# Kernel tuning notes

Hardware: AMD Instinct MI355X
Metric: run time of the kernel (lower is better)

The kernel has to match this reference:

```python
import jax, jax.numpy as jnp
import numpy as np

EMBED_DIM = 1024
NUM_HEADS = 16
HEAD_DIM = EMBED_DIM // NUM_HEADS


def setup_inputs() -> dict:
    key = jax.random.key(0)
    k1, k2, k3, k4 = jax.random.split(key, 4)
    S, B = 2048, 2
    x = jax.random.normal(k1, (S, B, EMBED_DIM), dtype=jnp.float32)
    # xavier_uniform for in_proj_weight [3E, E]
    limit_in = float(np.sqrt(6.0 / (3 * EMBED_DIM + EMBED_DIM)))
    in_proj_weight = jax.random.uniform(k2, (3 * EMBED_DIM, EMBED_DIM), minval=-limit_in, maxval=limit_in, dtype=jnp.float32)
    in_proj_bias = jnp.zeros((3 * EMBED_DIM,), dtype=jnp.float32)
    # out_proj: nn.Linear default init (kaiming-uniform-ish); use uniform of similar scale
    limit_out = float(np.sqrt(1.0 / EMBED_DIM))
    out_proj_weight = jax.random.uniform(k3, (EMBED_DIM, EMBED_DIM), minval=-limit_out, maxval=limit_out, dtype=jnp.float32)
    out_proj_bias = jnp.zeros((EMBED_DIM,), dtype=jnp.float32)
    return {
        "x": x,
        "in_proj_weight": in_proj_weight,
        "in_proj_bias": in_proj_bias,
        "out_proj_weight": out_proj_weight,
        "out_proj_bias": out_proj_bias,
    }


def reference(x, in_proj_weight, in_proj_bias, out_proj_weight, out_proj_bias):
    S, B, E = x.shape
    H, D = NUM_HEADS, HEAD_DIM
    scaling = float(D) ** -0.5
    # fused QKV projection: [S, B, 3E]
    qkv = jnp.einsum("sbe,fe->sbf", x, in_proj_weight) + in_proj_bias
    q, k, v = jnp.split(qkv, 3, axis=-1)
    q = q * scaling
    # [S, B, E] -> [B*H, S, D]
    def to_heads(t):
        return t.reshape(S, B * H, D).transpose(1, 0, 2)
    q, k, v = to_heads(q), to_heads(k), to_heads(v)
    # attention scores [B*H, S, S]
    scores = jnp.einsum("btd,bsd->bts", q, k)
    weights = jax.nn.softmax(scores, axis=-1)
    # dropout p=0.0 -> identity
    attn = jnp.einsum("bts,bsd->btd", weights, v)  # [B*H, S, D]
    attn = attn.transpose(1, 0, 2).reshape(S, B, E)
    out = jnp.einsum("sbe,fe->sbf", attn, out_proj_weight) + out_proj_bias
    return out
```

## Files before the change

kernel.cpp:

```cpp
#include <hip/hip_runtime.h>

typedef __bf16 bf16_t;
typedef __attribute__((ext_vector_type(8))) __bf16 bf16x8;
typedef __attribute__((ext_vector_type(4))) __bf16 bf16x4;
typedef __attribute__((ext_vector_type(4))) float f32x4;

#define MFMA16(a, b, c) __builtin_amdgcn_mfma_f32_16x16x32_bf16((a), (b), (c), 0, 0, 0)
#define LOG2E 1.44269504088896f

__device__ __forceinline__ void async16(const bf16_t* g, bf16_t* l) {
    __builtin_amdgcn_global_load_lds(
        (const __attribute__((address_space(1))) unsigned int*)g,
        (__attribute__((address_space(3))) unsigned int*)l, 16, 0, 0);
}

__global__ __launch_bounds__(256) void conv3(
    const float* __restrict__ s0, const float* __restrict__ s1,
    const float* __restrict__ s2, bf16_t* __restrict__ dst,
    int n0, int n1)
{
    const int i = (blockIdx.x * 256 + threadIdx.x) * 8;
    const float* src;
    int off;
    if (i < n0)           { src = s0; off = 0; }
    else if (i < n0 + n1) { src = s1; off = n0; }
    else                  { src = s2; off = n0 + n1; }
    const float4 a = *reinterpret_cast<const float4*>(src + i - off);
    const float4 b = *reinterpret_cast<const float4*>(src + i - off + 4);
    bf16x8 o;
    o[0] = (bf16_t)a.x; o[1] = (bf16_t)a.y; o[2] = (bf16_t)a.z; o[3] = (bf16_t)a.w;
    o[4] = (bf16_t)b.x; o[5] = (bf16_t)b.y; o[6] = (bf16_t)b.z; o[7] = (bf16_t)b.w;
    *reinterpret_cast<bf16x8*>(dst + i) = o;
}

template <int MT, bool F32OUT>
__global__ __launch_bounds__(256) void gemm_nt_lds(
    const bf16_t* __restrict__ W, const bf16_t* __restrict__ X,
    const float* __restrict__ bias, void* __restrict__ Cv,
    int N, int K, int scale_lim, float qscale)
{
    constexpr int NJ = MT / 32;
    __shared__ bf16_t As[128 * 64];
    __shared__ bf16_t Bs[MT * 64];

    const int lane = threadIdx.x & 63;
    const int wv   = threadIdx.x >> 6;
    const int l15  = lane & 15;
    const int qd   = lane >> 4;

    const int fb = blockIdx.x * 128;
    const int mb = blockIdx.y * MT;
    const int fw = (wv & 1) * 64;
    const int mw = (wv >> 1) * (MT / 2);

    f32x4 acc[4][NJ] = {};

    for (int k0 = 0; k0 < K; k0 += 64) {
        __syncthreads();
#pragma unroll
        for (int t = 0; t < 4; t++) {
            const int p = wv * 256 + t * 64 + lane;
            const int r = p >> 3, cg = (p & 7) ^ (r & 7);
            async16(W + (size_t)(fb + r) * K + k0 + cg * 8,
                    As + (wv * 256 + t * 64) * 8);
        }
#pragma unroll
        for (int t = 0; t < MT / 32; t++) {
            const int p = wv * (MT * 2) + t * 64 + lane;
            const int r = p >> 3, cg = (p & 7) ^ (r & 7);
            async16(X + (size_t)(mb + r) * K + k0 + cg * 8,
                    Bs + (wv * (MT * 2) + t * 64) * 8);
        }
        __syncthreads();

        const int s7 = l15 & 7;
#pragma unroll
        for (int ks = 0; ks < 2; ks++) {
            bf16x8 a[4], bfr[NJ];
#pragma unroll
            for (int i = 0; i < 4; i++) {
                const int r = fw + i * 16 + l15;
                a[i] = *reinterpret_cast<const bf16x8*>(
                    As + r * 64 + (((ks * 4 + qd) ^ s7) * 8));
            }
#pragma unroll
            for (int j = 0; j < NJ; j++) {
                const int r = mw + j * 16 + l15;
                bfr[j] = *reinterpret_cast<const bf16x8*>(
                    Bs + r * 64 + (((ks * 4 + qd) ^ s7) * 8));
            }
#pragma unroll
            for (int i = 0; i < 4; i++)
#pragma unroll
                for (int j = 0; j < NJ; j++)
                    acc[i][j] = MFMA16(a[i], bfr[j], acc[i][j]);
        }
    }

    const float scale = (fb < scale_lim) ? qscale : 1.0f;
#pragma unroll
    for (int i = 0; i < 4; i++) {
        const int f0 = fb + fw + i * 16 + qd * 4;
        float bs[4];
#pragma unroll
        for (int r = 0; r < 4; r++) bs[r] = bias[f0 + r];
#pragma unroll
        for (int j = 0; j < NJ; j++) {
            const int m = mb + mw + j * 16 + l15;
            if (F32OUT) {
                float4 o;
                o.x = (acc[i][j][0] + bs[0]) * scale;
                o.y = (acc[i][j][1] + bs[1]) * scale;
                o.z = (acc[i][j][2] + bs[2]) * scale;
                o.w = (acc[i][j][3] + bs[3]) * scale;
                *reinterpret_cast<float4*>((float*)Cv + (size_t)m * N + f0) = o;
            } else {
                bf16x4 o;
#pragma unroll
                for (int r = 0; r < 4; r++)
                    o[r] = (bf16_t)((acc[i][j][r] + bs[r]) * scale);
                *reinterpret_cast<bf16x4*>((bf16_t*)Cv + (size_t)m * N + f0) = o;
            }
        }
    }
}

__global__ __launch_bounds__(256) void flash_attn(
    const bf16_t* __restrict__ qkv, bf16_t* __restrict__ attn,
    int S, int B)
{
    const int E3 = 3072, E = 1024;
    const int b  = blockIdx.x >> 4;
    const int h  = blockIdx.x & 15;
    const int lane = threadIdx.x & 63;
    const int wv   = threadIdx.x >> 6;
    const int l15  = lane & 15;
    const int qd   = lane >> 4;

    __shared__ bf16_t Kt[128 * 64];
    __shared__ bf16_t VtS[64 * 128];
    __shared__ bf16_t Psh[4][16 * 128];

    const int qrow = blockIdx.y * 64 + wv * 16 + l15;
    const bf16_t* qp = qkv + (size_t)(qrow * B + b) * E3 + h * 64 + qd * 8;
    const bf16x8 qf0 = *reinterpret_cast<const bf16x8*>(qp);
    const bf16x8 qf1 = *reinterpret_cast<const bf16x8*>(qp + 32);

    bf16x8 ones;
#pragma unroll
    for (int j = 0; j < 8; j++) ones[j] = (bf16_t)1.0f;

    f32x4 oacc[4] = {};
    f32x4 lacc = {};

    const int tp = threadIdx.x & 31;
    const int tc = threadIdx.x >> 5;

    for (int kv0 = 0; kv0 < S; kv0 += 128) {
        __syncthreads();
#pragma unroll
        for (int t = 0; t < 4; t++) {
            const int p = wv * 256 + t * 64 + lane;
            const int r = p >> 3, cg = (p & 7) ^ (r & 7);
            async16(qkv + (size_t)((kv0 + r) * B + b) * E3 + E + h * 64 + cg * 8,
                    Kt + (wv * 256 + t * 64) * 8);
        }
#pragma unroll
        for (int pass = 0; pass < 2; pass++) {
            const int n0 = pass * 64 + 2 * tp;
            const bf16_t* vp0 = qkv + (size_t)((kv0 + n0) * B + b) * E3 + 2 * E + h * 64 + tc * 8;
            const bf16_t* vp1 = vp0 + (size_t)B * E3;
            bf16x8 v0 = *reinterpret_cast<const bf16x8*>(vp0);
            bf16x8 v1 = *reinterpret_cast<const bf16x8*>(vp1);
            const int cc = n0 >> 3;
            const int co = n0 & 7;
#pragma unroll
            for (int j = 0; j < 8; j++) {
                const int d = tc * 8 + j;
                union { bf16_t e[2]; unsigned u; } pk;
                pk.e[0] = v0[j]; pk.e[1] = v1[j];
                *reinterpret_cast<unsigned*>(&VtS[d * 128 + (cc ^ (d & 15)) * 8 + co]) = pk.u;
            }
        }
        __syncthreads();

        f32x4 st[8];
        const int s7 = l15 & 7;
        const int pc0 = qd ^ s7;
#pragma unroll
        for (int nt = 0; nt < 8; nt++) {
            const int r = nt * 16 + l15;
            bf16x8 kf0 = *reinterpret_cast<const bf16x8*>(Kt + r * 64 + pc0 * 8);
            bf16x8 kf1 = *reinterpret_cast<const bf16x8*>(Kt + r * 64 + (pc0 ^ 4) * 8);
            f32x4 c = {};
            c = MFMA16(kf0, qf0, c);
            st[nt] = MFMA16(kf1, qf1, c);
        }

        bf16_t* pw = &Psh[wv][0];
#pragma unroll
        for (int nt = 0; nt < 8; nt++) {
            bf16x4 pq;
#pragma unroll
            for (int r = 0; r < 4; r++)
                pq[r] = (bf16_t)__builtin_amdgcn_exp2f(st[nt][r]);
            const int c = nt * 2 + (qd >> 1);
            *reinterpret_cast<bf16x4*>(&pw[l15 * 128 + ((c ^ l15) * 8) + (qd & 1) * 4]) = pq;
        }

#pragma unroll
        for (int ks = 0; ks < 4; ks++) {
            const int pc = (ks * 4 + qd) ^ l15;
            bf16x8 pf = *reinterpret_cast<const bf16x8*>(&pw[l15 * 128 + pc * 8]);
            lacc = MFMA16(ones, pf, lacc);
#pragma unroll
            for (int dt = 0; dt < 4; dt++) {
                bf16x8 vf = *reinterpret_cast<const bf16x8*>(&VtS[(dt * 16 + l15) * 128 + pc * 8]);
                oacc[dt] = MFMA16(vf, pf, oacc[dt]);
            }
        }
    }

    const float inv = 1.0f / lacc[0];
#pragma unroll
    for (int dt = 0; dt < 4; dt++) {
        bf16x4 o;
#pragma unroll
        for (int r = 0; r < 4; r++) o[r] = (bf16_t)(oacc[dt][r] * inv);
        *reinterpret_cast<bf16x4*>(attn + (size_t)(qrow * B + b) * E +
                                   h * 64 + dt * 16 + qd * 4) = o;
    }
}

extern "C" void kernel_launch(void* const* d_in, const int* in_sizes, int n_in,
                              void* d_out, int out_size, void* d_ws, size_t ws_size,
                              hipStream_t stream) {
    const float* x  = (const float*)d_in[0];
    const float* wi = (const float*)d_in[1];
    const float* bi = (const float*)d_in[2];
    const float* wo = (const float*)d_in[3];
    const float* bo = (const float*)d_in[4];
    float* out = (float*)d_out;

    const int S = 2048, B = 2, E = 1024;
    const int M = S * B;

    bf16_t* xb   = (bf16_t*)d_ws;
    bf16_t* wib  = xb  + (size_t)M * E;
    bf16_t* wob  = wib + (size_t)3 * E * E;
    bf16_t* qkv  = wob + (size_t)E * E;
    bf16_t* attn = qkv + (size_t)M * 3 * E;

    const int n0 = M * E, n1 = 3 * E * E, n2 = E * E;
    conv3<<<(n0 + n1 + n2) / 8 / 256, 256, 0, stream>>>(x, wi, wo, xb, n0, n1);

    gemm_nt_lds<128, false><<<dim3(3 * E / 128, M / 128), 256, 0, stream>>>(
        wib, xb, bi, qkv, 3 * E, E, E, 0.125f * LOG2E);

    flash_attn<<<dim3(B * 16, S / 64), 256, 0, stream>>>(qkv, attn, S, B);

    gemm_nt_lds<64, true><<<dim3(E / 128, M / 64), 256, 0, stream>>>(
        wob, attn, bo, out, E, E, 0, 1.0f);
}
```

Before: 217.4 us.

## Rewrite flash attention with 32x32 MFMA, 2 waves per block, register P shuffle

Each wave now handles 32 query rows with 32x32x16 bf16 MFMA instead of 16 rows with 16x16x32, and the block shrinks from 4 waves to 2 for the same 64 queries. The probability tile no longer goes through shared memory; it is rearranged into the B-operand layout with cross-half lane shuffles. The aim is to cut LDS traffic and MFMA issue count per output. The cost is fewer waves per block for latency hiding, more K/V loading work per thread, and higher register pressure from the 16-wide accumulators.

```diff
diff --git a/kernel.cpp b/kernel.cpp
--- a/kernel.cpp
+++ b/kernel.cpp
@@ -4,14 +4,22 @@
 typedef __attribute__((ext_vector_type(8))) __bf16 bf16x8;
 typedef __attribute__((ext_vector_type(4))) __bf16 bf16x4;
 typedef __attribute__((ext_vector_type(4))) float f32x4;
+typedef __attribute__((ext_vector_type(16))) float f32x16;
 
 #define MFMA16(a, b, c) __builtin_amdgcn_mfma_f32_16x16x32_bf16((a), (b), (c), 0, 0, 0)
+#define MFMA32(a, b, c) __builtin_amdgcn_mfma_f32_32x32x16_bf16((a), (b), (c), 0, 0, 0)
 #define LOG2E 1.44269504088896f
 
 __device__ __forceinline__ void async16(const bf16_t* g, bf16_t* l) {
     __builtin_amdgcn_global_load_lds(
         (const __attribute__((address_space(1))) unsigned int*)g,
         (__attribute__((address_space(3))) unsigned int*)l, 16, 0, 0);
+}
+
+__device__ __forceinline__ unsigned pack2(float a, float b) {
+    union { bf16_t e[2]; unsigned u; } x;
+    x.e[0] = (bf16_t)a; x.e[1] = (bf16_t)b;
+    return x.u;
 }
 
 __global__ __launch_bounds__(256) void conv3(
@@ -125,111 +133,122 @@
     }
 }
 
-__global__ __launch_bounds__(256) void flash_attn(
+__global__ __launch_bounds__(128) void flash_attn(
     const bf16_t* __restrict__ qkv, bf16_t* __restrict__ attn,
     int S, int B)
 {
     const int E3 = 3072, E = 1024;
     const int b  = blockIdx.x >> 4;
     const int h  = blockIdx.x & 15;
-    const int lane = threadIdx.x & 63;
-    const int wv   = threadIdx.x >> 6;
-    const int l15  = lane & 15;
-    const int qd   = lane >> 4;
+    const int tid  = threadIdx.x;
+    const int lane = tid & 63;
+    const int wv   = tid >> 6;
+    const int l31  = lane & 31;
+    const int half = lane >> 5;
 
     __shared__ bf16_t Kt[128 * 64];
-    __shared__ bf16_t VtS[64 * 128];
-    __shared__ bf16_t Psh[4][16 * 128];
-
-    const int qrow = blockIdx.y * 64 + wv * 16 + l15;
-    const bf16_t* qp = qkv + (size_t)(qrow * B + b) * E3 + h * 64 + qd * 8;
-    const bf16x8 qf0 = *reinterpret_cast<const bf16x8*>(qp);
-    const bf16x8 qf1 = *reinterpret_cast<const bf16x8*>(qp + 32);
+    __shared__ bf16_t Vt[64 * 128];
+
+    const int qrow = blockIdx.y * 64 + wv * 32 + l31;
+    const bf16_t* qp = qkv + (size_t)(qrow * B + b) * E3 + h * 64;
+    bf16x8 qf[4];
+#pragma unroll
+    for (int ks = 0; ks < 4; ks++)
+        qf[ks] = *reinterpret_cast<const bf16x8*>(qp + ks * 16 + half * 8);
 
     bf16x8 ones;
 #pragma unroll
     for (int j = 0; j < 8; j++) ones[j] = (bf16_t)1.0f;
 
-    f32x4 oacc[4] = {};
-    f32x4 lacc = {};
-
-    const int tp = threadIdx.x & 31;
-    const int tc = threadIdx.x >> 5;
+    f32x16 oacc[2] = {};
+    f32x16 lacc = {};
 
     for (int kv0 = 0; kv0 < S; kv0 += 128) {
         __syncthreads();
 #pragma unroll
-        for (int t = 0; t < 4; t++) {
-            const int p = wv * 256 + t * 64 + lane;
+        for (int t = 0; t < 8; t++) {
+            const int p = wv * 512 + t * 64 + lane;
             const int r = p >> 3, cg = (p & 7) ^ (r & 7);
             async16(qkv + (size_t)((kv0 + r) * B + b) * E3 + E + h * 64 + cg * 8,
-                    Kt + (wv * 256 + t * 64) * 8);
-        }
-#pragma unroll
-        for (int pass = 0; pass < 2; pass++) {
-            const int n0 = pass * 64 + 2 * tp;
-            const bf16_t* vp0 = qkv + (size_t)((kv0 + n0) * B + b) * E3 + 2 * E + h * 64 + tc * 8;
-            const bf16_t* vp1 = vp0 + (size_t)B * E3;
-            bf16x8 v0 = *reinterpret_cast<const bf16x8*>(vp0);
-            bf16x8 v1 = *reinterpret_cast<const bf16x8*>(vp1);
-            const int cc = n0 >> 3;
-            const int co = n0 & 7;
-#pragma unroll
-            for (int j = 0; j < 8; j++) {
-                const int d = tc * 8 + j;
-                union { bf16_t e[2]; unsigned u; } pk;
-                pk.e[0] = v0[j]; pk.e[1] = v1[j];
-                *reinterpret_cast<unsigned*>(&VtS[d * 128 + (cc ^ (d & 15)) * 8 + co]) = pk.u;
-            }
-        }
-        __syncthreads();
-
-        f32x4 st[8];
-        const int s7 = l15 & 7;
-        const int pc0 = qd ^ s7;
-#pragma unroll
-        for (int nt = 0; nt < 8; nt++) {
-            const int r = nt * 16 + l15;
-            bf16x8 kf0 = *reinterpret_cast<const bf16x8*>(Kt + r * 64 + pc0 * 8);
-            bf16x8 kf1 = *reinterpret_cast<const bf16x8*>(Kt + r * 64 + (pc0 ^ 4) * 8);
-            f32x4 c = {};
-            c = MFMA16(kf0, qf0, c);
-            st[nt] = MFMA16(kf1, qf1, c);
-        }
-
-        bf16_t* pw = &Psh[wv][0];
-#pragma unroll
-        for (int nt = 0; nt < 8; nt++) {
-            bf16x4 pq;
-#pragma unroll
-            for (int r = 0; r < 4; r++)
-                pq[r] = (bf16_t)__builtin_amdgcn_exp2f(st[nt][r]);
-            const int c = nt * 2 + (qd >> 1);
-            *reinterpret_cast<bf16x4*>(&pw[l15 * 128 + ((c ^ l15) * 8) + (qd & 1) * 4]) = pq;
-        }
-
-#pragma unroll
-        for (int ks = 0; ks < 4; ks++) {
-            const int pc = (ks * 4 + qd) ^ l15;
-            bf16x8 pf = *reinterpret_cast<const bf16x8*>(&pw[l15 * 128 + pc * 8]);
-            lacc = MFMA16(ones, pf, lacc);
-#pragma unroll
-            for (int dt = 0; dt < 4; dt++) {
-                bf16x8 vf = *reinterpret_cast<const bf16x8*>(&VtS[(dt * 16 + l15) * 128 + pc * 8]);
-                oacc[dt] = MFMA16(vf, pf, oacc[dt]);
+                    Kt + (wv * 512 + t * 64) * 8);
+        }
+        {
+            const int n0 = 2 * (tid & 63);
+            const int cc = n0 >> 3, co = n0 & 7;
+#pragma unroll
+            for (int pass = 0; pass < 4; pass++) {
+                const int dc = pass * 2 + (tid >> 6);
+                const bf16_t* vp0 = qkv + (size_t)((kv0 + n0) * B + b) * E3 + 2 * E + h * 64 + dc * 8;
+                const bf16_t* vp1 = vp0 + (size_t)B * E3;
+                bf16x8 v0 = *reinterpret_cast<const bf16x8*>(vp0);
+                bf16x8 v1 = *reinterpret_cast<const bf16x8*>(vp1);
+#pragma unroll
+                for (int j = 0; j < 8; j++) {
+                    const int d = dc * 8 + j;
+                    *reinterpret_cast<unsigned*>(
+                        &Vt[d * 128 + ((cc ^ (d & 15)) * 8) + co]) = pack2((float)v0[j], (float)v1[j]);
+                }
+            }
+        }
+        __syncthreads();
+
+#pragma unroll
+        for (int nt = 0; nt < 4; nt++) {
+            f32x16 st = {};
+            const int r = nt * 32 + l31;
+            const int r7 = r & 7;
+#pragma unroll
+            for (int ks = 0; ks < 4; ks++) {
+                bf16x8 kf = *reinterpret_cast<const bf16x8*>(
+                    Kt + r * 64 + (((ks * 2 + half) ^ r7) * 8));
+                st = MFMA32(kf, qf[ks], st);
+            }
+            unsigned q8[8];
+#pragma unroll
+            for (int g = 0; g < 4; g++) {
+                q8[2 * g]     = pack2(__builtin_amdgcn_exp2f(st[4 * g]),
+                                      __builtin_amdgcn_exp2f(st[4 * g + 1]));
+                q8[2 * g + 1] = pack2(__builtin_amdgcn_exp2f(st[4 * g + 2]),
+                                      __builtin_amdgcn_exp2f(st[4 * g + 3]));
+            }
+            unsigned x8[8];
+#pragma unroll
+            for (int k = 0; k < 8; k++) x8[k] = __shfl_xor((int)q8[k], 32);
+            union { unsigned u[4]; bf16x8 v; } pf[2];
+            pf[0].u[0] = half ? x8[2] : q8[0];
+            pf[0].u[1] = half ? x8[3] : q8[1];
+            pf[0].u[2] = half ? q8[2] : x8[0];
+            pf[0].u[3] = half ? q8[3] : x8[1];
+            pf[1].u[0] = half ? x8[6] : q8[4];
+            pf[1].u[1] = half ? x8[7] : q8[5];
+            pf[1].u[2] = half ? q8[6] : x8[4];
+            pf[1].u[3] = half ? q8[7] : x8[5];
+#pragma unroll
+            for (int t = 0; t < 2; t++) {
+                lacc = MFMA32(ones, pf[t].v, lacc);
+                const int c = nt * 4 + t * 2 + half;
+#pragma unroll
+                for (int dt = 0; dt < 2; dt++) {
+                    const int d = dt * 32 + l31;
+                    bf16x8 vf = *reinterpret_cast<const bf16x8*>(
+                        Vt + d * 128 + ((c ^ (d & 15)) * 8));
+                    oacc[dt] = MFMA32(vf, pf[t].v, oacc[dt]);
+                }
             }
         }
     }
 
     const float inv = 1.0f / lacc[0];
 #pragma unroll
-    for (int dt = 0; dt < 4; dt++) {
-        bf16x4 o;
-#pragma unroll
-        for (int r = 0; r < 4; r++) o[r] = (bf16_t)(oacc[dt][r] * inv);
-        *reinterpret_cast<bf16x4*>(attn + (size_t)(qrow * B + b) * E +
-                                   h * 64 + dt * 16 + qd * 4) = o;
-    }
+    for (int dt = 0; dt < 2; dt++)
+#pragma unroll
+        for (int g = 0; g < 4; g++) {
+            bf16x4 o;
+#pragma unroll
+            for (int r = 0; r < 4; r++) o[r] = (bf16_t)(oacc[dt][4 * g + r] * inv);
+            *reinterpret_cast<bf16x4*>(attn + (size_t)(qrow * B + b) * E +
+                                       h * 64 + dt * 32 + g * 8 + half * 4) = o;
+        }
 }
 
 extern "C" void kernel_launch(void* const* d_in, const int* in_sizes, int n_in,
@@ -257,7 +276,7 @@
     gemm_nt_lds<128, false><<<dim3(3 * E / 128, M / 128), 256, 0, stream>>>(
         wib, xb, bi, qkv, 3 * E, E, E, 0.125f * LOG2E);
 
-    flash_attn<<<dim3(B * 16, S / 64), 256, 0, stream>>>(qkv, attn, S, B);
+    flash_attn<<<dim3(B * 16, S / 64), 128, 0, stream>>>(qkv, attn, S, B);
 
     gemm_nt_lds<64, true><<<dim3(E / 128, M / 64), 256, 0, stream>>>(
         wob, attn, bo, out, E, E, 0, 1.0f);
```

After: 229.2 us. 5.4% more time.
